# Performance work log

Hardware: AMD Instinct MI355X
Metric: run time of the kernel (lower is better)

The kernel has to match this reference:

```python
import jax, jax.numpy as jnp
import numpy as np

N = 20000
E = 320000
IN_F = 128
HEADS = 8
OUT_F = 32
NEG_SLOPE = 0.2


def setup_inputs() -> dict:
    key = jax.random.key(0)
    k = jax.random.split(key, 8)
    x = jax.random.normal(k[0], (N, IN_F), dtype=jnp.float32)
    edge_index = jax.random.randint(k[1], (2, E), 0, N, dtype=jnp.int32)
    # Linear weights stored torch-style: [out, in]
    scale = 1.0 / np.sqrt(IN_F)
    W = jax.random.normal(k[2], (HEADS * OUT_F, IN_F), dtype=jnp.float32) * scale
    W1 = jax.random.normal(k[3], (HEADS * OUT_F, IN_F), dtype=jnp.float32) * scale
    W2 = jax.random.normal(k[4], (HEADS * OUT_F, IN_F), dtype=jnp.float32) * scale
    att = jax.random.normal(k[5], (1, HEADS, OUT_F), dtype=jnp.float32) * 0.1
    bias = jnp.zeros((HEADS * OUT_F,), dtype=jnp.float32)
    return {"x": x, "edge_index": edge_index, "W": W, "W1": W1, "W2": W2,
            "att": att, "bias": bias}


def reference(x, edge_index, W, W1, W2, att, bias):
    n, heads, out_f = x.shape[0], att.shape[1], att.shape[2]
    src, dst = edge_index[0], edge_index[1]

    # Node projections: [N, H, F]
    h_src = (x @ W1.T).reshape(n, heads, out_f)
    h_dst = (x @ W2.T).reshape(n, heads, out_f)
    values = (x @ W.T).reshape(n, heads, out_f)

    # Edge-wise GATv2 logits: a^T LeakyReLU(W1 h_i + W2 h_j)  -> [E, H]
    att_input = jax.nn.leaky_relu(h_src[src] + h_dst[dst], negative_slope=NEG_SLOPE)
    logits = jnp.einsum('ehf,hf->eh', att_input, att[0])

    # Segment softmax over incoming edges of each dst node (stable).
    seg_max = jax.ops.segment_max(logits, dst, num_segments=n)  # [N, H]
    exp_l = jnp.exp(logits - seg_max[dst])
    denom = jax.ops.segment_sum(exp_l, dst, num_segments=n)     # [N, H]
    weights = exp_l / denom[dst]                                # [E, H]

    # Weighted aggregation of source values into dst nodes.
    weighted = weights[:, :, None] * values[src]                # [E, H, F]
    out = jax.ops.segment_sum(weighted, dst, num_segments=n)    # [N, H, F]

    out = out.reshape(n, heads * out_f) + bias
    return out
```

## Files before the change

kernel.cpp:

```cpp
#include <hip/hip_runtime.h>
#include <math.h>

#define NN 20000
#define EE 320000
#define KF 128
#define HO 256
#define CAP 96

typedef __attribute__((ext_vector_type(8))) short short8;
typedef __attribute__((ext_vector_type(4))) float f32x4;

static __device__ __forceinline__ unsigned short f2bf(float f) {
    union { float f; unsigned u; } v; v.f = f;
    unsigned u = v.u;
    u += 0x7fffu + ((u >> 16) & 1u);
    return (unsigned short)(u >> 16);
}
static __device__ __forceinline__ float bf2f(unsigned short b) {
    union { unsigned u; float f; } v; v.u = ((unsigned)b) << 16;
    return v.f;
}

__global__ __launch_bounds__(256) void prep_kernel(
    const float* __restrict__ x, const float* __restrict__ W0,
    const float* __restrict__ W1, const float* __restrict__ W2,
    unsigned short* __restrict__ xb, unsigned short* __restrict__ wb,
    int* __restrict__ cursor)
{
    const int b = blockIdx.x;
    const int t = threadIdx.x;
    if (b < 96) {
        const int m = b >> 5;
        const float* __restrict__ Wm = (m == 0) ? W0 : (m == 1) ? W1 : W2;
        int idx = (b & 31) * 1024 + t * 4;
        float4 v = *(const float4*)(Wm + idx);
        ushort4 o;
        o.x = f2bf(v.x); o.y = f2bf(v.y); o.z = f2bf(v.z); o.w = f2bf(v.w);
        *(ushort4*)(wb + (size_t)m * 32768 + idx) = o;
    } else if (b < 2596) {
        size_t i = (size_t)(b - 96) * 1024 + t * 4;
        float4 v = *(const float4*)(x + i);
        ushort4 o;
        o.x = f2bf(v.x); o.y = f2bf(v.y); o.z = f2bf(v.z); o.w = f2bf(v.w);
        *(ushort4*)(xb + i) = o;
    } else {
        int i = (b - 2596) * 256 + t;
        if (i < NN) cursor[i] = 0;
    }
}

__global__ void scatter_kernel(const int* __restrict__ ei, int* __restrict__ cursor,
                               int* __restrict__ csr_src) {
    int e = blockIdx.x * blockDim.x + threadIdx.x;
    if (e < EE) {
        int s = ei[e];
        int d = ei[EE + e];
        int pos = atomicAdd(&cursor[d], 1);
        if (pos < CAP) csr_src[d * CAP + pos] = s;
    }
}

__global__ __launch_bounds__(256, 3) void proj_kernel(
    const unsigned short* __restrict__ xb, const unsigned short* __restrict__ wb,
    unsigned short* __restrict__ hv, unsigned short* __restrict__ hdst)
{
    __shared__ unsigned short lds[4][16][256];

    const int m = blockIdx.y;
    const unsigned short* __restrict__ Wm = wb + (size_t)m * 32768;
    unsigned short* __restrict__ dst = (m == 0) ? (hv + 256) : (m == 1) ? hv : hdst;
    const int stride = (m == 2) ? 256 : 512;

    const int w    = threadIdx.x >> 6;
    const int lane = threadIdx.x & 63;
    const int lr   = lane & 15;
    const int q    = lane >> 4;
    const int r0   = blockIdx.x * 64 + w * 16;

    f32x4 acc[16];
#pragma unroll
    for (int nt = 0; nt < 16; ++nt) acc[nt] = (f32x4){0.f, 0.f, 0.f, 0.f};

#pragma unroll
    for (int ks = 0; ks < 4; ++ks) {
        const int kcol = ks * 32 + q * 8;
        const int arow = r0 + lr;
        short8 a_f = (short8){0,0,0,0,0,0,0,0};
        if (arow < NN) a_f = *(const short8*)(xb + (size_t)arow * KF + kcol);
#pragma unroll
        for (int nt = 0; nt < 16; ++nt) {
            short8 b_f = *(const short8*)(Wm + (size_t)(nt * 16 + lr) * KF + kcol);
            acc[nt] = __builtin_amdgcn_mfma_f32_16x16x32_bf16(a_f, b_f, acc[nt], 0, 0, 0);
        }
    }

#pragma unroll
    for (int nt = 0; nt < 16; ++nt)
#pragma unroll
        for (int r = 0; r < 4; ++r)
            lds[w][q * 4 + r][nt * 16 + lr] = f2bf(acc[nt][r]);
    __syncthreads();

    const int half = lane >> 5;
    const int xoff = (lane & 31) * 8;
#pragma unroll
    for (int it = 0; it < 8; ++it) {
        const int rl = it * 2 + half;
        const int r  = r0 + rl;
        if (r < NN) {
            short8 v = *(const short8*)&lds[w][rl][xoff];
            *(short8*)(dst + (size_t)r * stride + xoff) = v;
        }
    }
}

__global__ __launch_bounds__(128) void gat_kernel(
    const unsigned short* __restrict__ hv, const unsigned short* __restrict__ hdst,
    const float* __restrict__ att, const float* __restrict__ bias,
    const int* __restrict__ cursor, const int* __restrict__ csr_src,
    float* __restrict__ out)
{
    const int w    = threadIdx.x >> 6;
    const int d    = blockIdx.x * 2 + w;
    const int lane = threadIdx.x & 63;
    const int col  = lane * 4;

    const float4 a4 = *(const float4*)(att + col);
    const float4 b4 = *(const float4*)(bias + col);
    const ushort4 hd4 = *(const ushort4*)(hdst + (size_t)d * HO + col);
    const float hd0 = bf2f(hd4.x), hd1 = bf2f(hd4.y), hd2 = bf2f(hd4.z), hd3 = bf2f(hd4.w);

    int deg = cursor[d];
    if (deg > CAP) deg = CAP;

    int sreg = (lane < deg) ? csr_src[d * CAP + lane] : 0;

    float l = 0.f;
    float o0 = 0.f, o1 = 0.f, o2 = 0.f, o3 = 0.f;

#define EDGE_CALC(HV, VV)                                                     \
    {                                                                         \
        float z0 = bf2f(HV.x) + hd0, z1 = bf2f(HV.y) + hd1;                   \
        float z2 = bf2f(HV.z) + hd2, z3 = bf2f(HV.w) + hd3;                   \
        z0 = fmaxf(z0, 0.2f * z0); z1 = fmaxf(z1, 0.2f * z1);                 \
        z2 = fmaxf(z2, 0.2f * z2); z3 = fmaxf(z3, 0.2f * z3);                 \
        float p = fmaf(a4.x, z0, a4.y * z1) + fmaf(a4.z, z2, a4.w * z3);      \
        p += __shfl_xor(p, 1); p += __shfl_xor(p, 2); p += __shfl_xor(p, 4);  \
        const float e = __expf(p);                                            \
        l += e;                                                               \
        o0 = fmaf(e, bf2f(VV.x), o0);                                         \
        o1 = fmaf(e, bf2f(VV.y), o1);                                         \
        o2 = fmaf(e, bf2f(VV.z), o2);                                         \
        o3 = fmaf(e, bf2f(VV.w), o3);                                         \
    }

    const int nfast = (deg < 64) ? deg : 64;
    int i = 0;
    for (; i + 4 <= nfast; i += 4) {
        const int s0 = __shfl(sreg, i);
        const int s1 = __shfl(sreg, i + 1);
        const int s2 = __shfl(sreg, i + 2);
        const int s3 = __shfl(sreg, i + 3);
        const unsigned short* p0 = hv + (size_t)s0 * 512 + col;
        const unsigned short* p1 = hv + (size_t)s1 * 512 + col;
        const unsigned short* p2 = hv + (size_t)s2 * 512 + col;
        const unsigned short* p3 = hv + (size_t)s3 * 512 + col;
        const ushort4 hv0 = *(const ushort4*)p0;
        const ushort4 vv0 = *(const ushort4*)(p0 + 256);
        const ushort4 hv1 = *(const ushort4*)p1;
        const ushort4 vv1 = *(const ushort4*)(p1 + 256);
        const ushort4 hv2 = *(const ushort4*)p2;
        const ushort4 vv2 = *(const ushort4*)(p2 + 256);
        const ushort4 hv3 = *(const ushort4*)p3;
        const ushort4 vv3 = *(const ushort4*)(p3 + 256);
        EDGE_CALC(hv0, vv0);
        EDGE_CALC(hv1, vv1);
        EDGE_CALC(hv2, vv2);
        EDGE_CALC(hv3, vv3);
    }
    for (; i < nfast; ++i) {
        const int s0 = __shfl(sreg, i);
        const unsigned short* p0 = hv + (size_t)s0 * 512 + col;
        const ushort4 hv0 = *(const ushort4*)p0;
        const ushort4 vv0 = *(const ushort4*)(p0 + 256);
        EDGE_CALC(hv0, vv0);
    }
    for (int j = 64; j < deg; ++j) {
        const int s0 = csr_src[d * CAP + j];
        const unsigned short* p0 = hv + (size_t)s0 * 512 + col;
        const ushort4 hv0 = *(const ushort4*)p0;
        const ushort4 vv0 = *(const ushort4*)(p0 + 256);
        EDGE_CALC(hv0, vv0);
    }
#undef EDGE_CALC

    const float inv = (deg > 0) ? 1.f / l : 0.f;
    float4 res;
    res.x = o0 * inv + b4.x;
    res.y = o1 * inv + b4.y;
    res.z = o2 * inv + b4.z;
    res.w = o3 * inv + b4.w;
    *(float4*)(out + (size_t)d * HO + col) = res;
}

extern "C" void kernel_launch(void* const* d_in, const int* in_sizes, int n_in,
                              void* d_out, int out_size, void* d_ws, size_t ws_size,
                              hipStream_t stream) {
    const float* x    = (const float*)d_in[0];
    const int*   ei   = (const int*)d_in[1];
    const float* W0   = (const float*)d_in[2];
    const float* W1   = (const float*)d_in[3];
    const float* W2   = (const float*)d_in[4];
    const float* att  = (const float*)d_in[5];
    const float* bias = (const float*)d_in[6];
    float* out = (float*)d_out;

    char* p = (char*)d_ws;
    unsigned short* hv   = (unsigned short*)p; p += (size_t)NN * 512 * 2;
    unsigned short* hdst = (unsigned short*)p; p += (size_t)NN * HO * 2;
    unsigned short* xb   = (unsigned short*)p; p += (size_t)NN * KF * 2;
    unsigned short* wb   = (unsigned short*)p; p += (size_t)3 * 32768 * 2;
    int* cursor  = (int*)p; p += (size_t)NN * sizeof(int);
    int* csr_src = (int*)p; p += (size_t)NN * CAP * sizeof(int);

    prep_kernel<<<2675, 256, 0, stream>>>(x, W0, W1, W2, xb, wb, cursor);
    scatter_kernel<<<(EE + 255) / 256, 256, 0, stream>>>(ei, cursor, csr_src);
    proj_kernel<<<dim3(313, 3), 256, 0, stream>>>(xb, wb, hv, hdst);
    gat_kernel<<<NN / 2, 128, 0, stream>>>(hv, hdst, att, bias, cursor, csr_src, out);
}
```

Before: 176.2 us.

## Keep weight fragments in registers per wave and drop LDS staging in projection

Each wave now owns a 64-column slice of the output and preloads its weight fragments into registers once. It then iterates over four 16-row tiles of x, instead of loading all 256 weight columns per k-step for a single 16-row tile. The LDS transpose buffer and barrier are removed, and results are written directly as scattered 2-byte stores. Fewer accumulators raise the occupancy target, but the uncoalesced narrow global stores may cost more than the LDS-staged vector stores did.

```diff
diff --git a/kernel.cpp b/kernel.cpp
--- a/kernel.cpp
+++ b/kernel.cpp
@@ -60,12 +60,10 @@
     }
 }
 
-__global__ __launch_bounds__(256, 3) void proj_kernel(
+__global__ __launch_bounds__(256, 4) void proj_kernel(
     const unsigned short* __restrict__ xb, const unsigned short* __restrict__ wb,
     unsigned short* __restrict__ hv, unsigned short* __restrict__ hdst)
 {
-    __shared__ unsigned short lds[4][16][256];
-
     const int m = blockIdx.y;
     const unsigned short* __restrict__ Wm = wb + (size_t)m * 32768;
     unsigned short* __restrict__ dst = (m == 0) ? (hv + 256) : (m == 1) ? hv : hdst;
@@ -75,41 +73,48 @@
     const int lane = threadIdx.x & 63;
     const int lr   = lane & 15;
     const int q    = lane >> 4;
-    const int r0   = blockIdx.x * 64 + w * 16;
-
-    f32x4 acc[16];
-#pragma unroll
-    for (int nt = 0; nt < 16; ++nt) acc[nt] = (f32x4){0.f, 0.f, 0.f, 0.f};
-
-#pragma unroll
-    for (int ks = 0; ks < 4; ++ks) {
-        const int kcol = ks * 32 + q * 8;
+    const int cb   = w * 64;
+
+    short8 Bf[4][4];
+#pragma unroll
+    for (int nt = 0; nt < 4; ++nt)
+#pragma unroll
+        for (int ks = 0; ks < 4; ++ks)
+            Bf[nt][ks] = *(const short8*)(Wm + (size_t)(cb + nt * 16 + lr) * KF + ks * 32 + q * 8);
+
+    const int rb = blockIdx.x * 64;
+
+#pragma unroll
+    for (int it = 0; it < 4; ++it) {
+        const int r0 = rb + it * 16;
+
+        short8 Af[4];
         const int arow = r0 + lr;
-        short8 a_f = (short8){0,0,0,0,0,0,0,0};
-        if (arow < NN) a_f = *(const short8*)(xb + (size_t)arow * KF + kcol);
-#pragma unroll
-        for (int nt = 0; nt < 16; ++nt) {
-            short8 b_f = *(const short8*)(Wm + (size_t)(nt * 16 + lr) * KF + kcol);
-            acc[nt] = __builtin_amdgcn_mfma_f32_16x16x32_bf16(a_f, b_f, acc[nt], 0, 0, 0);
+#pragma unroll
+        for (int ks = 0; ks < 4; ++ks) {
+            Af[ks] = (short8){0,0,0,0,0,0,0,0};
+            if (arow < NN)
+                Af[ks] = *(const short8*)(xb + (size_t)arow * KF + ks * 32 + q * 8);
         }
-    }
-
-#pragma unroll
-    for (int nt = 0; nt < 16; ++nt)
-#pragma unroll
-        for (int r = 0; r < 4; ++r)
-            lds[w][q * 4 + r][nt * 16 + lr] = f2bf(acc[nt][r]);
-    __syncthreads();
-
-    const int half = lane >> 5;
-    const int xoff = (lane & 31) * 8;
-#pragma unroll
-    for (int it = 0; it < 8; ++it) {
-        const int rl = it * 2 + half;
-        const int r  = r0 + rl;
-        if (r < NN) {
-            short8 v = *(const short8*)&lds[w][rl][xoff];
-            *(short8*)(dst + (size_t)r * stride + xoff) = v;
+
+        f32x4 acc[4];
+#pragma unroll
+        for (int nt = 0; nt < 4; ++nt) acc[nt] = (f32x4){0.f, 0.f, 0.f, 0.f};
+
+#pragma unroll
+        for (int ks = 0; ks < 4; ++ks)
+#pragma unroll
+            for (int nt = 0; nt < 4; ++nt)
+                acc[nt] = __builtin_amdgcn_mfma_f32_16x16x32_bf16(Af[ks], Bf[nt][ks], acc[nt], 0, 0, 0);
+
+#pragma unroll
+        for (int nt = 0; nt < 4; ++nt) {
+#pragma unroll
+            for (int r = 0; r < 4; ++r) {
+                const int row = r0 + q * 4 + r;
+                if (row < NN)
+                    dst[(size_t)row * stride + cb + nt * 16 + lr] = f2bf(acc[nt][r]);
+            }
         }
     }
 }
```

Measured after the change: 161.6 us. -8.3%, faster.
